# Kernel tuning notes

Hardware: AMD Instinct MI355X
Metric: run time of the kernel (lower is better)

Reference implementation:

```python
import jax, jax.numpy as jnp
import numpy as np

B, T, C = 2, 2048, 2048
N_HEAD, N_GROUP = 32, 8
HEAD_DIM = C // N_HEAD           # 64
HIG = N_HEAD // N_GROUP          # heads per group = 4


def setup_inputs() -> dict:
    key = jax.random.key(0)
    ks = jax.random.split(key, 8)
    s = 1.0 / np.sqrt(C)
    return {
        "q": jax.random.normal(ks[0], (B, T, C), jnp.float32),
        "k": jax.random.normal(ks[1], (B, T, C), jnp.float32),
        "v": jax.random.normal(ks[2], (B, T, C), jnp.float32),
        "Wq": jax.random.normal(ks[3], (C, C), jnp.float32) * s,
        "Wk": jax.random.normal(ks[4], (N_GROUP * HEAD_DIM, C), jnp.float32) * s,
        "Wv": jax.random.normal(ks[5], (N_GROUP * HEAD_DIM, C), jnp.float32) * s,
        "Wp": jax.random.normal(ks[6], (C, C), jnp.float32) * s,
        "bp": jax.random.normal(ks[7], (C,), jnp.float32) * s,
    }


def reference(q, k, v, Wq, Wk, Wv, Wp, bp):
    # Q projection -> (B, HIG, G, T, D); head h = i*G + g (row-major split of n_head)
    qp = (q @ Wq.T).reshape(B, T, N_HEAD, HEAD_DIM)
    qp = qp.transpose(0, 2, 1, 3).reshape(B, HIG, N_GROUP, T, HEAD_DIM)
    # K/V projections -> (B, G, T, D), shared across heads within a group
    kp = (k @ Wk.T).reshape(B, T, N_GROUP, HEAD_DIM).transpose(0, 2, 1, 3)
    vp = (v @ Wv.T).reshape(B, T, N_GROUP, HEAD_DIM).transpose(0, 2, 1, 3)
    scale = 1.0 / jnp.sqrt(jnp.asarray(HEAD_DIM, qp.dtype))
    scores = jnp.einsum('bigtd,bgsd->bigts', qp, kp) * scale  # (B,HIG,G,T,T)
    attn = jax.nn.softmax(scores, axis=-1)
    out = jnp.einsum('bigts,bgsd->bigtd', attn, vp)           # (B,HIG,G,T,D)
    out = out.reshape(B, N_HEAD, T, HEAD_DIM).transpose(0, 2, 1, 3).reshape(B, T, C)
    return out @ Wp.T + bp  # dropout is identity in eval mode
```

## Files before the change

kernel.cpp:

```cpp
#include <hip/hip_runtime.h>

#define DEVI __device__ __forceinline__

typedef __bf16 bf16_t;
typedef __bf16 bf16x8 __attribute__((ext_vector_type(8)));
typedef __bf16 bf16x4v __attribute__((ext_vector_type(4)));
typedef float f32x4 __attribute__((ext_vector_type(4)));

#define CSL 0.18033688011112042f

#if __has_builtin(__builtin_amdgcn_exp2f)
DEVI float fast_exp2(float x) { return __builtin_amdgcn_exp2f(x); }
#else
DEVI float fast_exp2(float x) {
  float r;
  asm volatile("v_exp_f32 %0, %1\n\ts_nop 1" : "=v"(r) : "v"(x));
  return r;
}
#endif

DEVI void async16(void* lds, const void* g) {
  __builtin_amdgcn_global_load_lds(
      (const __attribute__((address_space(1))) unsigned int*)g,
      (__attribute__((address_space(3))) unsigned int*)lds, 16, 0, 0);
}

__global__ __launch_bounds__(256) void cvt3(const float* __restrict__ a,
                                            const float* __restrict__ b,
                                            const float* __restrict__ c,
                                            bf16_t* __restrict__ da,
                                            bf16_t* __restrict__ db,
                                            bf16_t* __restrict__ dc, int n) {
  const float* s = (blockIdx.y == 0) ? a : (blockIdx.y == 1) ? b : c;
  bf16_t* d = (blockIdx.y == 0) ? da : (blockIdx.y == 1) ? db : dc;
  const int i = (blockIdx.x * 256 + threadIdx.x) * 4;
  if (i < n) {
    const float4 f = *(const float4*)(s + i);
    bf16x4v o;
    o.x = (bf16_t)f.x; o.y = (bf16_t)f.y; o.z = (bf16_t)f.z; o.w = (bf16_t)f.w;
    *(bf16x4v*)(d + i) = o;
  }
}
__global__ __launch_bounds__(256) void cvt2(const float* __restrict__ a,
                                            const float* __restrict__ b,
                                            bf16_t* __restrict__ da,
                                            bf16_t* __restrict__ db, int n) {
  const float* s = (blockIdx.y == 0) ? a : b;
  bf16_t* d = (blockIdx.y == 0) ? da : db;
  const int i = (blockIdx.x * 256 + threadIdx.x) * 4;
  if (i < n) {
    const float4 f = *(const float4*)(s + i);
    bf16x4v o;
    o.x = (bf16_t)f.x; o.y = (bf16_t)f.y; o.z = (bf16_t)f.z; o.w = (bf16_t)f.w;
    *(bf16x4v*)(d + i) = o;
  }
}

template<int MODE>
DEVI void gemm_core(const bf16_t* __restrict__ A, const bf16_t* __restrict__ W,
                    const float* __restrict__ bias, void* __restrict__ outv,
                    int N, int K, int bx, int by)
{
  __shared__ __align__(16) bf16_t Al[128 * 32];
  __shared__ __align__(16) bf16_t Bl[128 * 32];
  const int t = threadIdx.x;
  const int w = t >> 6, lane = t & 63;
  const int l15 = lane & 15, quad = lane >> 4;
  const int wm = (w >> 1) * 64, wn = (w & 1) * 64;
  const int m0 = by * 128, n0 = bx * 128;
  const int srow = t >> 2;
  const int skc = (t & 3) * 8;

  f32x4 acc[4][4] = {};

  for (int kk = 0; kk < K; kk += 32) {
    __syncthreads();
#pragma unroll
    for (int i = 0; i < 2; ++i) {
      async16(Al + i * 2048 + w * 512,
              A + (size_t)(m0 + i * 64 + srow) * K + kk + skc);
      async16(Bl + i * 2048 + w * 512,
              W + (size_t)(n0 + i * 64 + srow) * K + kk + skc);
    }
    __syncthreads();
    bf16x8 af[4], bfr[4];
#pragma unroll
    for (int x = 0; x < 4; ++x) {
      af[x]  = *(const bf16x8*)&Al[(wm + x * 16 + l15) * 32 + quad * 8];
      bfr[x] = *(const bf16x8*)&Bl[(wn + x * 16 + l15) * 32 + quad * 8];
    }
#pragma unroll
    for (int mt = 0; mt < 4; ++mt)
#pragma unroll
      for (int nt = 0; nt < 4; ++nt)
        acc[mt][nt] = __builtin_amdgcn_mfma_f32_16x16x32_bf16(af[mt], bfr[nt], acc[mt][nt], 0, 0, 0);
  }

#pragma unroll
  for (int mt = 0; mt < 4; ++mt) {
#pragma unroll
    for (int nt = 0; nt < 4; ++nt) {
      const int n = n0 + wn + nt * 16 + l15;
#pragma unroll
      for (int r = 0; r < 4; ++r) {
        const int m = m0 + wm + mt * 16 + quad * 4 + r;
        const float v = acc[mt][nt][r];
        if (MODE == 0) {
          ((bf16_t*)outv)[(size_t)m * N + n] = (bf16_t)v;
        } else if (MODE == 1) {
          ((float*)outv)[(size_t)m * N + n] = v + bias[n];
        } else if (MODE == 2) {
          ((bf16_t*)outv)[(size_t)(m >> 11) * (512 * 2048) + (size_t)n * 2048 + (m & 2047)] = (bf16_t)v;
        } else {
          ((bf16_t*)outv)[(size_t)m * N + n] = (bf16_t)(v * CSL);
        }
      }
    }
  }
}

__global__ __launch_bounds__(256) void gemm_scaled(const bf16_t* __restrict__ A,
                                                   const bf16_t* __restrict__ W,
                                                   bf16_t* __restrict__ out, int N, int K) {
  gemm_core<3>(A, W, nullptr, out, N, K, blockIdx.x, blockIdx.y);
}
__global__ __launch_bounds__(256) void gemm_bias_f32(const bf16_t* __restrict__ A,
                                                     const bf16_t* __restrict__ W,
                                                     const float* __restrict__ bias,
                                                     float* __restrict__ out, int N, int K) {
  gemm_core<1>(A, W, bias, out, N, K, blockIdx.x, blockIdx.y);
}
__global__ __launch_bounds__(256) void gemm_kv(const bf16_t* __restrict__ kin,
                                               const bf16_t* __restrict__ Wk,
                                               bf16_t* __restrict__ kp,
                                               const bf16_t* __restrict__ vin,
                                               const bf16_t* __restrict__ Wv,
                                               bf16_t* __restrict__ vt) {
  if (blockIdx.z == 0) gemm_core<0>(kin, Wk, nullptr, kp, 512, 2048, blockIdx.x, blockIdx.y);
  else                 gemm_core<2>(vin, Wv, nullptr, vt, 512, 2048, blockIdx.x, blockIdx.y);
}

__global__ __launch_bounds__(256) void attn_kernel(
    const bf16_t* __restrict__ Qp, const bf16_t* __restrict__ Kp,
    const bf16_t* __restrict__ Vt, bf16_t* __restrict__ O)
{
  __shared__ __align__(16) bf16_t Kl[64 * 64];
  __shared__ __align__(16) bf16_t Vl[2][64 * 64];
  __shared__ __align__(16) bf16_t Pl[4 * 32 * 64];

  const int t = threadIdx.x;
  const int w = t >> 6, lane = t & 63;
  const int l15 = lane & 15, quad = lane >> 4;
  const int h = blockIdx.y, b = blockIdx.z, g = h & 7;
  const int t0 = blockIdx.x * 128 + w * 32;

  const size_t qbase = (size_t)b * (2048u * 2048u) + (size_t)h * 64;
  const size_t kbase = (size_t)b * (2048u * 512u) + (size_t)g * 64;
  const size_t vbase = (size_t)b * (512u * 2048u) + (size_t)(g * 64) * 2048u;

  bf16x8 qf[2][2];
#pragma unroll
  for (int nt = 0; nt < 2; ++nt)
#pragma unroll
    for (int kc = 0; kc < 2; ++kc)
      qf[nt][kc] = *(const bf16x8*)&Qp[qbase + (size_t)(t0 + nt * 16 + l15) * 2048 + kc * 32 + quad * 8];

  f32x4 oacc[2][4] = {};
  f32x4 rs4[2] = {};

  const int xk = l15 & 7;
  const int xp = ((l15 & 7) << 1) | (l15 >> 3);
  const int pbase = w << 11;

  const int lrow = lane >> 3;
  const int lchk = (lane & 7) ^ lrow;
  const bf16_t* ksrc = Kp + kbase + (size_t)(w * 8 + lrow) * 512 + lchk * 8;
  const bf16_t* vsrc = Vt + vbase + (size_t)(w * 8 + lrow) * 2048 + lchk * 8;

#pragma unroll
  for (int i = 0; i < 2; ++i) {
    async16(&Kl[(i * 32 + w * 8) * 64], ksrc + (size_t)(i * 32) * 512);
    async16(&Vl[0][(i * 32 + w * 8) * 64], vsrc + (size_t)(i * 32) * 2048);
  }

  for (int it = 0; it < 32; ++it) {
    const int cur = it & 1;
    __syncthreads();

    if (it < 31) {
      const int s1 = (it + 1) * 64;
#pragma unroll
      for (int i = 0; i < 2; ++i)
        async16(&Vl[cur ^ 1][(i * 32 + w * 8) * 64], vsrc + (size_t)(i * 32) * 2048 + s1);
    }

    f32x4 sacc[4][2] = {};
#pragma unroll
    for (int kc = 0; kc < 2; ++kc) {
#pragma unroll
      for (int kt = 0; kt < 4; ++kt) {
        bf16x8 kf = *(const bf16x8*)&Kl[((kt * 16 + l15) << 6) + (((kc * 4 + quad) ^ xk) << 3)];
        __builtin_amdgcn_s_setprio(1);
#pragma unroll
        for (int nt = 0; nt < 2; ++nt)
          sacc[kt][nt] = __builtin_amdgcn_mfma_f32_16x16x32_bf16(kf, qf[nt][kc], sacc[kt][nt], 0, 0, 0);
        __builtin_amdgcn_s_setprio(0);
      }
    }

    __syncthreads();

    if (it < 31) {
      const int s1 = (it + 1) * 64;
#pragma unroll
      for (int i = 0; i < 2; ++i)
        async16(&Kl[(i * 32 + w * 8) * 64], ksrc + (size_t)(s1 + i * 32) * 512);
    }

#pragma unroll
    for (int nt = 0; nt < 2; ++nt) {
#pragma unroll
      for (int kt = 0; kt < 4; ++kt) {
        const float p0 = fast_exp2(sacc[kt][nt][0]);
        const float p1 = fast_exp2(sacc[kt][nt][1]);
        const float p2 = fast_exp2(sacc[kt][nt][2]);
        const float p3 = fast_exp2(sacc[kt][nt][3]);
        f32x4 pv; pv[0] = p0; pv[1] = p1; pv[2] = p2; pv[3] = p3;
        rs4[nt] += pv;
        bf16x4v o;
        o.x = (bf16_t)p0; o.y = (bf16_t)p1; o.z = (bf16_t)p2; o.w = (bf16_t)p3;
        *(bf16x4v*)&Pl[pbase + ((nt * 16 + l15) << 6) + (((kt * 4 + quad) ^ xp) << 2)] = o;
      }
    }

#pragma unroll
    for (int kc = 0; kc < 2; ++kc) {
      bf16x8 pf[2];
#pragma unroll
      for (int mt = 0; mt < 2; ++mt) {
        const int rb = pbase + ((mt * 16 + l15) << 6);
        bf16x4v plo = *(const bf16x4v*)&Pl[rb + (((kc * 8 + quad * 2)     ^ xp) << 2)];
        bf16x4v phi = *(const bf16x4v*)&Pl[rb + (((kc * 8 + quad * 2 + 1) ^ xp) << 2)];
        pf[mt] = __builtin_shufflevector(plo, phi, 0, 1, 2, 3, 4, 5, 6, 7);
      }
#pragma unroll
      for (int db = 0; db < 4; ++db) {
        bf16x8 vf = *(const bf16x8*)&Vl[cur][((db * 16 + l15) << 6) + (((kc * 4 + quad) ^ xk) << 3)];
        __builtin_amdgcn_s_setprio(1);
#pragma unroll
        for (int mt = 0; mt < 2; ++mt)
          oacc[mt][db] = __builtin_amdgcn_mfma_f32_16x16x32_bf16(pf[mt], vf, oacc[mt][db], 0, 0, 0);
        __builtin_amdgcn_s_setprio(0);
      }
    }
  }

  float linv[2][4];
#pragma unroll
  for (int nt = 0; nt < 2; ++nt) {
    float rl = (rs4[nt][0] + rs4[nt][1]) + (rs4[nt][2] + rs4[nt][3]);
    rl += __shfl_xor(rl, 16);
    rl += __shfl_xor(rl, 32);
#pragma unroll
    for (int r = 0; r < 4; ++r)
      linv[nt][r] = 1.0f / __shfl(rl, quad * 4 + r);
  }

#pragma unroll
  for (int mt = 0; mt < 2; ++mt)
#pragma unroll
    for (int db = 0; db < 4; ++db)
#pragma unroll
      for (int r = 0; r < 4; ++r) {
        const int tt = t0 + mt * 16 + quad * 4 + r;
        const int d = db * 16 + l15;
        O[((size_t)(b * 2048 + tt) * 32 + h) * 64 + d] = (bf16_t)(oacc[mt][db][r] * linv[mt][r]);
      }
}

extern "C" void kernel_launch(void* const* d_in, const int* in_sizes, int n_in,
                              void* d_out, int out_size, void* d_ws, size_t ws_size,
                              hipStream_t stream) {
  const float* q  = (const float*)d_in[0];
  const float* k  = (const float*)d_in[1];
  const float* v  = (const float*)d_in[2];
  const float* Wq = (const float*)d_in[3];
  const float* Wk = (const float*)d_in[4];
  const float* Wv = (const float*)d_in[5];
  const float* Wp = (const float*)d_in[6];
  const float* bp = (const float*)d_in[7];
  float* out = (float*)d_out;

  bf16_t* ws = (bf16_t*)d_ws;
  bf16_t* qb  = ws;
  bf16_t* kb  = ws +  8388608;
  bf16_t* vb  = ws + 16777216;
  bf16_t* Wqb = ws + 25165824;
  bf16_t* Wkb = ws + 29360128;
  bf16_t* Wvb = ws + 30408704;
  bf16_t* Wpb = ws + 31457280;
  bf16_t* Qp  = ws + 35651584;
  bf16_t* Kp  = ws + 44040192;
  bf16_t* Vt  = ws + 46137344;
  bf16_t* Ob  = qb;

  cvt3<<<dim3(8192, 3), 256, 0, stream>>>(q, k, v, qb, kb, vb, 8388608);
  cvt2<<<dim3(4096, 2), 256, 0, stream>>>(Wq, Wp, Wqb, Wpb, 4194304);
  cvt2<<<dim3(1024, 2), 256, 0, stream>>>(Wk, Wv, Wkb, Wvb, 1048576);

  gemm_scaled<<<dim3(16, 32), 256, 0, stream>>>(qb, Wqb, Qp, 2048, 2048);
  gemm_kv<<<dim3(4, 32, 2), 256, 0, stream>>>(kb, Wkb, Kp, vb, Wvb, Vt);
  attn_kernel<<<dim3(16, 32, 2), 256, 0, stream>>>(Qp, Kp, Vt, Ob);
  gemm_bias_f32<<<dim3(16, 32), 256, 0, stream>>>(Ob, Wpb, bp, out, 2048, 2048);
}
```

Before: 428.5 us.

## Replace async global-to-LDS K/V loads with register-staged prefetch

The direct global_load_lds async copies of K and V tiles are replaced by a register prefetch. The next tile is loaded into registers during the current iteration, then written to a single swizzled LDS buffer after a barrier. This drops the V double buffer and moves the K reload point, so each iteration now uses two barriers around the LDS store. It trades fewer LDS bytes for extra VGPRs and explicit LDS write instructions. It also relies on the register loads covering latency across a full iteration.

```diff
diff --git a/kernel.cpp b/kernel.cpp
--- a/kernel.cpp
+++ b/kernel.cpp
@@ -145,7 +145,7 @@
     const bf16_t* __restrict__ Vt, bf16_t* __restrict__ O)
 {
   __shared__ __align__(16) bf16_t Kl[64 * 64];
-  __shared__ __align__(16) bf16_t Vl[2][64 * 64];
+  __shared__ __align__(16) bf16_t Vl[64 * 64];
   __shared__ __align__(16) bf16_t Pl[4 * 32 * 64];
 
   const int t = threadIdx.x;
@@ -172,27 +172,39 @@
   const int xp = ((l15 & 7) << 1) | (l15 >> 3);
   const int pbase = w << 11;
 
-  const int lrow = lane >> 3;
-  const int lchk = (lane & 7) ^ lrow;
-  const bf16_t* ksrc = Kp + kbase + (size_t)(w * 8 + lrow) * 512 + lchk * 8;
-  const bf16_t* vsrc = Vt + vbase + (size_t)(w * 8 + lrow) * 2048 + lchk * 8;
-
+  const int srow = t >> 3;
+  const int sc8 = (t & 7) * 8;
+  const int swz = (((t & 7) ^ (srow & 7)) << 3);
+
+  bf16x8 kreg[2], vreg[2];
 #pragma unroll
   for (int i = 0; i < 2; ++i) {
-    async16(&Kl[(i * 32 + w * 8) * 64], ksrc + (size_t)(i * 32) * 512);
-    async16(&Vl[0][(i * 32 + w * 8) * 64], vsrc + (size_t)(i * 32) * 2048);
+    const int row = i * 32 + srow;
+    kreg[i] = *(const bf16x8*)&Kp[kbase + (size_t)row * 512 + sc8];
+    vreg[i] = *(const bf16x8*)&Vt[vbase + (size_t)row * 2048 + sc8];
   }
 
   for (int it = 0; it < 32; ++it) {
-    const int cur = it & 1;
     __syncthreads();
+
+#pragma unroll
+    for (int i = 0; i < 2; ++i) {
+      const int row = i * 32 + srow;
+      *(bf16x8*)&Kl[(row << 6) + swz] = kreg[i];
+      *(bf16x8*)&Vl[(row << 6) + swz] = vreg[i];
+    }
 
     if (it < 31) {
       const int s1 = (it + 1) * 64;
 #pragma unroll
-      for (int i = 0; i < 2; ++i)
-        async16(&Vl[cur ^ 1][(i * 32 + w * 8) * 64], vsrc + (size_t)(i * 32) * 2048 + s1);
-    }
+      for (int i = 0; i < 2; ++i) {
+        const int row = i * 32 + srow;
+        kreg[i] = *(const bf16x8*)&Kp[kbase + (size_t)(s1 + row) * 512 + sc8];
+        vreg[i] = *(const bf16x8*)&Vt[vbase + (size_t)row * 2048 + s1 + sc8];
+      }
+    }
+
+    __syncthreads();
 
     f32x4 sacc[4][2] = {};
 #pragma unroll
@@ -206,15 +218,6 @@
           sacc[kt][nt] = __builtin_amdgcn_mfma_f32_16x16x32_bf16(kf, qf[nt][kc], sacc[kt][nt], 0, 0, 0);
         __builtin_amdgcn_s_setprio(0);
       }
-    }
-
-    __syncthreads();
-
-    if (it < 31) {
-      const int s1 = (it + 1) * 64;
-#pragma unroll
-      for (int i = 0; i < 2; ++i)
-        async16(&Kl[(i * 32 + w * 8) * 64], ksrc + (size_t)(s1 + i * 32) * 512);
     }
 
 #pragma unroll
@@ -245,7 +248,7 @@
       }
 #pragma unroll
       for (int db = 0; db < 4; ++db) {
-        bf16x8 vf = *(const bf16x8*)&Vl[cur][((db * 16 + l15) << 6) + (((kc * 4 + quad) ^ xk) << 3)];
+        bf16x8 vf = *(const bf16x8*)&Vl[((db * 16 + l15) << 6) + (((kc * 4 + quad) ^ xk) << 3)];
         __builtin_amdgcn_s_setprio(1);
 #pragma unroll
         for (int mt = 0; mt < 2; ++mt)
```

After: 427.2 us. Within noise of the previous version (-0.3%).
